# Kernel tuning notes

Measured on AMD Instinct MI355X. Metric: run time of the kernel, lower is better.

Reference implementation:

```python
import jax, jax.numpy as jnp
import numpy as np

B, T, D, H = 8, 512, 1024, 16
DH = D // H  # per-head feature dim (64)


def setup_inputs() -> dict:
    key = jax.random.key(0)
    ks = jax.random.split(key, 10)
    s = 1.0 / np.sqrt(DH)
    inp = {
        "X_data": jax.random.normal(ks[0], (B, T, D), dtype=jnp.float32),
        "mask": jnp.ones((B, T), dtype=jnp.int32),
        # per-head Q/K/V projections (each SelfAttention has its own d_h x d_h weights)
        "Wq": jax.random.normal(ks[1], (H, DH, DH), dtype=jnp.float32) * s,
        "bq": jnp.zeros((H, DH), dtype=jnp.float32),
        "Wk": jax.random.normal(ks[2], (H, DH, DH), dtype=jnp.float32) * s,
        "bk": jnp.zeros((H, DH), dtype=jnp.float32),
        "Wv": jax.random.normal(ks[3], (H, DH, DH), dtype=jnp.float32) * s,
        "bv": jnp.zeros((H, DH), dtype=jnp.float32),
        # AttentionFusion: linear on concatenated head outputs -> len_feature_new
        "Wf": jax.random.normal(ks[4], (D, D), dtype=jnp.float32) * (1.0 / np.sqrt(D)),
        "bf": jnp.zeros((D,), dtype=jnp.float32),
    }
    return inp


def reference(X_data, mask, Wq, bq, Wk, bk, Wv, bv, Wf, bf):
    # Split features into heads: [B, T, H, DH] (equal partitions since D % H == 0)
    Xh = X_data.reshape(B, T, H, DH)
    # Batched per-head projections (replaces the Python loop over heads)
    Q = jnp.einsum("bthd,hde->bhte", Xh, Wq) + bq[None, :, None, :]
    K = jnp.einsum("bthd,hde->bhte", Xh, Wk) + bk[None, :, None, :]
    V = jnp.einsum("bthd,hde->bhte", Xh, Wv) + bv[None, :, None, :]
    scale = 1.0 / jnp.sqrt(jnp.asarray(DH, dtype=Q.dtype))
    scores = jnp.einsum("bhqe,bhke->bhqk", Q, K) * scale  # [B, H, T, T]
    scores = jnp.where(mask[:, None, None, :] > 0, scores, jnp.asarray(-1e9, scores.dtype))
    att = jax.nn.softmax(scores, axis=-1)
    out = jnp.einsum("bhqk,bhke->bhqe", att, V)  # [B, H, T, DH]
    # Concatenate heads (same order as the per-head loop) and fuse
    out = out.transpose(0, 2, 1, 3).reshape(B, T, D)
    fused = out @ Wf + bf  # AttentionFusion linear
    return fused
```

## Files before the change

### kernel.cpp

```cpp
#include <hip/hip_runtime.h>
#include <math.h>

#define B 8
#define T 512
#define D 1024
#define H 16
#define DH 64

typedef __bf16 bf16;
typedef __attribute__((ext_vector_type(8))) __bf16 bf16x8;
typedef __attribute__((ext_vector_type(4))) __bf16 bf16x4;
typedef __attribute__((ext_vector_type(4))) float f32x4;

__device__ __forceinline__ void gld16(const void* g, void* l) {
    __builtin_amdgcn_global_load_lds(
        (const __attribute__((address_space(1))) void*)g,
        (__attribute__((address_space(3))) void*)l, 16, 0, 0);
}


#define EXP2SCALE 1.44269504088896f

__global__ __launch_bounds__(256) void prep_w(
    const float* __restrict__ Wq, const float* __restrict__ Wk,
    const float* __restrict__ Wv, const float* __restrict__ Wf,
    bf16* __restrict__ WqT, bf16* __restrict__ WkT,
    bf16* __restrict__ WvT, bf16* __restrict__ WfT)
{
    __shared__ bf16 Ts[64 * 72];
    const int blk = blockIdx.x, tid = threadIdx.x;
    if (blk < 48) {
        const int m = blk >> 4, h = blk & 15;
        const float* src = (m == 0 ? Wq : (m == 1 ? Wk : Wv)) + h * 4096;
        bf16* dst = (m == 0 ? WqT : (m == 1 ? WkT : WvT)) + h * 4096;
        for (int i = tid; i < 1024; i += 256) {
            const int d = i >> 4, eq = (i & 15) * 4;
            const float4 w = *(const float4*)(src + d * 64 + eq);
            Ts[(eq + 0) * 72 + d] = (bf16)w.x; Ts[(eq + 1) * 72 + d] = (bf16)w.y;
            Ts[(eq + 2) * 72 + d] = (bf16)w.z; Ts[(eq + 3) * 72 + d] = (bf16)w.w;
        }
        __syncthreads();
        for (int i = tid; i < 512; i += 256) {
            const int e = i >> 3, kc = (i & 7) * 8;
            *(bf16x8*)(dst + e * 64 + kc) = *(const bf16x8*)&Ts[e * 72 + kc];
        }
    } else {
        const int ti = blk - 48, k0 = (ti >> 4) * 64, n0 = (ti & 15) * 64;
        for (int i = tid; i < 1024; i += 256) {
            const int k = i >> 4, nq = (i & 15) * 4;
            const float4 w = *(const float4*)(Wf + (size_t)(k0 + k) * D + n0 + nq);
            Ts[(nq + 0) * 72 + k] = (bf16)w.x; Ts[(nq + 1) * 72 + k] = (bf16)w.y;
            Ts[(nq + 2) * 72 + k] = (bf16)w.z; Ts[(nq + 3) * 72 + k] = (bf16)w.w;
        }
        __syncthreads();
        for (int i = tid; i < 512; i += 256) {
            const int n = i >> 3, kc = (i & 7) * 8;
            *(bf16x8*)(WfT + (size_t)(n0 + n) * D + k0 + kc) = *(const bf16x8*)&Ts[n * 72 + kc];
        }
    }
}

__global__ __launch_bounds__(256, 2) void qkv_attn(
    const float* __restrict__ X, const int* __restrict__ mask,
    const bf16* __restrict__ WqT, const bf16* __restrict__ WkT,
    const bf16* __restrict__ WvT,
    const float* __restrict__ bq, const float* __restrict__ bk,
    const float* __restrict__ bv,
    bf16* __restrict__ Ob)
{
    __shared__ __align__(16) char smem[80384];
    bf16* Wks = (bf16*)(smem);
    bf16* Wvs = (bf16*)(smem + 8192);
    bf16* Pl  = (bf16*)(smem + 53248);
    bf16* Xkt = (bf16*)(smem + 71680);
    int*  msk = (int*)(smem + 79872);
    bf16* Wqs   = (bf16*)(smem + 16384);
    bf16* Xq    = Pl;
    bf16* Stage = Pl;
    bf16* Ostage = Pl;

    const int bh = blockIdx.x & 127, q0 = (blockIdx.x >> 7) * 128;
    const int b = bh >> 4, h = bh & 15;
    const int tid = threadIdx.x, wave = tid >> 6, lane = tid & 63;
    const int quad = lane >> 4, l15 = lane & 15;
    const int lr = lane >> 3, lc = lane & 7;
    const int csw = (lc ^ lr) * 8;
    (void)bk;

    const int pkrow = wave * 16 + (lane >> 2);
    const int pc0 = (lane & 3) * 2;

    float bqr[4], bvr[4];
#pragma unroll
    for (int nt = 0; nt < 4; ++nt) {
        bqr[nt] = bq[h * DH + nt * 16 + l15];
        bvr[nt] = bv[h * DH + nt * 16 + l15];
    }

    float4 px0, px1, px2, px3;
    {
        const float* src = X + (size_t)(b * T + pkrow) * D + h * DH + pc0 * 8;
        px0 = *(const float4*)src; px1 = *(const float4*)(src + 4);
        px2 = *(const float4*)(src + 8); px3 = *(const float4*)(src + 12);
    }
    int mreg = (tid < 64) ? mask[(size_t)b * T + tid] : 0;

    {
        const int r1 = wave * 16;
#pragma unroll
        for (int j = 0; j < 2; ++j) {
            gld16(WqT + (size_t)h * 4096 + (r1 + j * 8 + lr) * 64 + csw, &Wqs[(r1 + j * 8) * 64]);
            gld16(WkT + (size_t)h * 4096 + (r1 + j * 8 + lr) * 64 + csw, &Wks[(r1 + j * 8) * 64]);
            gld16(WvT + (size_t)h * 4096 + (r1 + j * 8 + lr) * 64 + csw, &Wvs[(r1 + j * 8) * 64]);
        }
    }
    for (int i = tid; i < 1024; i += 256) {
        const int row = i >> 3, c = i & 7;
        const float* src = X + (size_t)(b * T + q0 + row) * D + h * DH + c * 8;
        const float4 x0 = *(const float4*)src;
        const float4 x1 = *(const float4*)(src + 4);
        bf16x8 t;
        t[0] = (bf16)x0.x; t[1] = (bf16)x0.y; t[2] = (bf16)x0.z; t[3] = (bf16)x0.w;
        t[4] = (bf16)x1.x; t[5] = (bf16)x1.y; t[6] = (bf16)x1.z; t[7] = (bf16)x1.w;
        *(bf16x8*)&Xq[row * 64 + ((c ^ (row & 7)) * 8)] = t;
    }
    __syncthreads();

    {
        f32x4 accQ[2][4] = {};
#pragma unroll
        for (int ks = 0; ks < 2; ++ks) {
            bf16x8 af[2], bfr[4];
#pragma unroll
            for (int mt = 0; mt < 2; ++mt) {
                const int row = wave * 32 + mt * 16 + l15;
                af[mt] = *(const bf16x8*)&Xq[row * 64 + (((ks * 4 + quad) ^ (l15 & 7)) * 8)];
            }
#pragma unroll
            for (int nt = 0; nt < 4; ++nt)
                bfr[nt] = *(const bf16x8*)&Wqs[(nt * 16 + l15) * 64 + (((ks * 4 + quad) ^ (l15 & 7)) * 8)];
#pragma unroll
            for (int mt = 0; mt < 2; ++mt)
#pragma unroll
                for (int nt = 0; nt < 4; ++nt)
                    accQ[mt][nt] = __builtin_amdgcn_mfma_f32_16x16x32_bf16(af[mt], bfr[nt], accQ[mt][nt], 0, 0, 0);
        }
        __syncthreads();
        const float qs = 0.125f * EXP2SCALE;
#pragma unroll
        for (int mt = 0; mt < 2; ++mt)
#pragma unroll
            for (int nt = 0; nt < 4; ++nt)
#pragma unroll
                for (int reg = 0; reg < 4; ++reg)
                    Stage[(wave * 32 + mt * 16 + quad * 4 + reg) * 72 + nt * 16 + l15] =
                        (bf16)((accQ[mt][nt][reg] + bqr[nt]) * qs);
        __builtin_amdgcn_wave_barrier();
    }
    bf16x8 qf[2][2];
#pragma unroll
    for (int mt = 0; mt < 2; ++mt)
#pragma unroll
        for (int ks = 0; ks < 2; ++ks)
            qf[mt][ks] = *(const bf16x8*)&Stage[(wave * 32 + mt * 16 + l15) * 72 + ks * 32 + quad * 8];

    f32x4 acc[2][4] = {};
    float lst2[2] = {0.f, 0.f};

    for (int kt = 0; kt < 8; ++kt) {
        const int p = kt & 1;
        bf16* Ks  = (bf16*)(smem + 16384 + p * 9216);
        bf16* Vts = (bf16*)(smem + 34816 + p * 9216);

        {
            bf16x8 t0, t1;
            t0[0] = (bf16)px0.x; t0[1] = (bf16)px0.y; t0[2] = (bf16)px0.z; t0[3] = (bf16)px0.w;
            t0[4] = (bf16)px1.x; t0[5] = (bf16)px1.y; t0[6] = (bf16)px1.z; t0[7] = (bf16)px1.w;
            t1[0] = (bf16)px2.x; t1[1] = (bf16)px2.y; t1[2] = (bf16)px2.z; t1[3] = (bf16)px2.w;
            t1[4] = (bf16)px3.x; t1[5] = (bf16)px3.y; t1[6] = (bf16)px3.z; t1[7] = (bf16)px3.w;
            *(bf16x8*)&Xkt[pkrow * 64 + ((pc0 ^ (pkrow & 7)) * 8)] = t0;
            *(bf16x8*)&Xkt[pkrow * 64 + (((pc0 + 1) ^ (pkrow & 7)) * 8)] = t1;
            if (tid < 64) msk[p * 64 + tid] = mreg;
        }
        __builtin_amdgcn_wave_barrier();

        if (kt < 7) {
            const float* src = X + (size_t)(b * T + (kt + 1) * 64 + pkrow) * D + h * DH + pc0 * 8;
            px0 = *(const float4*)src; px1 = *(const float4*)(src + 4);
            px2 = *(const float4*)(src + 8); px3 = *(const float4*)(src + 12);
            if (tid < 64) mreg = mask[(size_t)b * T + (kt + 1) * 64 + tid];
        }

        {
            bf16x8 afkv[2];
#pragma unroll
            for (int ks = 0; ks < 2; ++ks)
                afkv[ks] = *(const bf16x8*)&Xkt[(wave * 16 + l15) * 64 + (((ks * 4 + quad) ^ (l15 & 7)) * 8)];
            f32x4 accK[4] = {}, accV[4] = {};
#pragma unroll
            for (int ks = 0; ks < 2; ++ks)
#pragma unroll
                for (int nt = 0; nt < 4; ++nt) {
                    const bf16x8 bk8 = *(const bf16x8*)&Wks[(nt * 16 + l15) * 64 + (((ks * 4 + quad) ^ (l15 & 7)) * 8)];
                    accK[nt] = __builtin_amdgcn_mfma_f32_16x16x32_bf16(bk8, afkv[ks], accK[nt], 0, 0, 0);
                    const bf16x8 bv8 = *(const bf16x8*)&Wvs[(nt * 16 + l15) * 64 + (((ks * 4 + quad) ^ (l15 & 7)) * 8)];
                    accV[nt] = __builtin_amdgcn_mfma_f32_16x16x32_bf16(afkv[ks], bv8, accV[nt], 0, 0, 0);
                }
#pragma unroll
            for (int nt = 0; nt < 4; ++nt) {
                bf16x4 kp;
#pragma unroll
                for (int reg = 0; reg < 4; ++reg) kp[reg] = (bf16)accK[nt][reg];
                *(bf16x4*)&Ks[(wave * 16 + l15) * 72 + nt * 16 + quad * 4] = kp;
                bf16x4 vp;
#pragma unroll
                for (int reg = 0; reg < 4; ++reg) vp[reg] = (bf16)accV[nt][reg];
                *(bf16x4*)&Vts[(nt * 16 + l15) * 72 + wave * 16 + quad * 4] = vp;
            }
        }
        __syncthreads();

        bf16* Plw = Pl + wave * (32 * 72);
        {
            bf16x8 kf[4][2];
#pragma unroll
            for (int nt = 0; nt < 4; ++nt)
#pragma unroll
                for (int ks = 0; ks < 2; ++ks)
                    kf[nt][ks] = *(const bf16x8*)&Ks[(nt * 16 + l15) * 72 + ks * 32 + quad * 8];
            int4 mv4[4];
#pragma unroll
            for (int nt = 0; nt < 4; ++nt)
                mv4[nt] = *(const int4*)&msk[p * 64 + nt * 16 + quad * 4];
#pragma unroll
            for (int mt = 0; mt < 2; ++mt) {
                f32x4 s[4] = {};
#pragma unroll
                for (int ks = 0; ks < 2; ++ks)
#pragma unroll
                    for (int nt = 0; nt < 4; ++nt)
                        s[nt] = __builtin_amdgcn_mfma_f32_16x16x32_bf16(kf[nt][ks], qf[mt][ks], s[nt], 0, 0, 0);
#pragma unroll
                for (int nt = 0; nt < 4; ++nt) {
                    bf16x4 pp;
                    const float p0 = (mv4[nt].x > 0) ? exp2f(s[nt][0]) : 0.f;
                    const float p1 = (mv4[nt].y > 0) ? exp2f(s[nt][1]) : 0.f;
                    const float p2 = (mv4[nt].z > 0) ? exp2f(s[nt][2]) : 0.f;
                    const float p3 = (mv4[nt].w > 0) ? exp2f(s[nt][3]) : 0.f;
                    lst2[mt] += (p0 + p1) + (p2 + p3);
                    pp[0] = (bf16)p0; pp[1] = (bf16)p1; pp[2] = (bf16)p2; pp[3] = (bf16)p3;
                    *(bf16x4*)&Plw[(mt * 16 + l15) * 72 + nt * 16 + quad * 4] = pp;
                }
            }
        }
        __builtin_amdgcn_wave_barrier();

#pragma unroll
        for (int kc = 0; kc < 2; ++kc) {
            const bf16x8 pf0 = *(const bf16x8*)&Plw[(l15) * 72 + kc * 32 + quad * 8];
            const bf16x8 pf1 = *(const bf16x8*)&Plw[(16 + l15) * 72 + kc * 32 + quad * 8];
#pragma unroll
            for (int nt = 0; nt < 4; ++nt) {
                const bf16x8 vf = *(const bf16x8*)&Vts[(nt * 16 + l15) * 72 + kc * 32 + quad * 8];
                acc[0][nt] = __builtin_amdgcn_mfma_f32_16x16x32_bf16(pf0, vf, acc[0][nt], 0, 0, 0);
                acc[1][nt] = __builtin_amdgcn_mfma_f32_16x16x32_bf16(pf1, vf, acc[1][nt], 0, 0, 0);
            }
        }
    }

    __builtin_amdgcn_wave_barrier();
    float inv_r[2][4];
#pragma unroll
    for (int mt = 0; mt < 2; ++mt) {
        float l = lst2[mt];
        l += __shfl_xor(l, 16);
        l += __shfl_xor(l, 32);
        const float inv = 1.f / l;
#pragma unroll
        for (int reg = 0; reg < 4; ++reg)
            inv_r[mt][reg] = __shfl(inv, (lane & 48) | (quad * 4 + reg));
    }
#pragma unroll
    for (int mt = 0; mt < 2; ++mt)
#pragma unroll
        for (int reg = 0; reg < 4; ++reg) {
            const int row = wave * 32 + mt * 16 + quad * 4 + reg;
#pragma unroll
            for (int nt = 0; nt < 4; ++nt)
                Ostage[row * 72 + nt * 16 + l15] =
                    (bf16)(acc[mt][nt][reg] * inv_r[mt][reg] + bvr[nt]);
        }
    __syncthreads();
    for (int i = tid; i < 1024; i += 256) {
        const int row = i >> 3, c = (i & 7) * 8;
        *(bf16x8*)(Ob + ((size_t)b * T + q0 + row) * D + h * DH + c) =
            *(const bf16x8*)&Ostage[row * 72 + c];
    }
}

__global__ __launch_bounds__(256, 2) void fuse_mfma(
    const bf16* __restrict__ Ob, const bf16* __restrict__ WfT,
    const float* __restrict__ bfv, float* __restrict__ out)
{
    __shared__ __align__(16) char smem[65536];

    const int col0 = blockIdx.x * 128;
    const int row0 = blockIdx.y * 128;
    const int tid = threadIdx.x, wave = tid >> 6, lane = tid & 63;
    const int quad = lane >> 4, l15 = lane & 15;
    const int lr = lane >> 3, lc = lane & 7;
    const int wm = wave * 32;

    f32x4 acc[2][8] = {};

    auto stage = [&](int k0, int buf) {
        bf16* As = (bf16*)(smem + buf * 16384);
        bf16* Bs = (bf16*)(smem + 32768 + buf * 16384);
#pragma unroll
        for (int j = 0; j < 4; ++j) {
            const int row = wm + j * 8 + lr;
            gld16(Ob + (size_t)(row0 + row) * D + k0 + ((lc ^ (row & 7)) * 8),
                  &As[(wm + j * 8) * 64]);
            gld16(WfT + (size_t)(col0 + row) * D + k0 + ((lc ^ (row & 7)) * 8),
                  &Bs[(wm + j * 8) * 64]);
        }
    };

    stage(0, 0);
    __syncthreads();

    for (int i = 0; i < 16; ++i) {
        const int buf = i & 1;
        if (i < 15) stage((i + 1) * 64, buf ^ 1);
        bf16* As = (bf16*)(smem + buf * 16384);
        bf16* Bs = (bf16*)(smem + 32768 + buf * 16384);
#pragma unroll
        for (int ks = 0; ks < 2; ++ks) {
            bf16x8 af[2], bfr[8];
#pragma unroll
            for (int mt = 0; mt < 2; ++mt) {
                const int row = wm + mt * 16 + l15;
                af[mt] = *(const bf16x8*)&As[row * 64 + (((ks * 4 + quad) ^ (l15 & 7)) * 8)];
            }
#pragma unroll
            for (int nt = 0; nt < 8; ++nt)
                bfr[nt] = *(const bf16x8*)&Bs[(nt * 16 + l15) * 64 + (((ks * 4 + quad) ^ (l15 & 7)) * 8)];
#pragma unroll
            for (int mt = 0; mt < 2; ++mt)
#pragma unroll
                for (int nt = 0; nt < 8; ++nt)
                    acc[mt][nt] = __builtin_amdgcn_mfma_f32_16x16x32_bf16(af[mt], bfr[nt], acc[mt][nt], 0, 0, 0);
        }
        __syncthreads();
    }

    float* Ofs = (float*)smem;
    float bias[8];
#pragma unroll
    for (int nt = 0; nt < 8; ++nt) bias[nt] = bfv[col0 + nt * 16 + l15];
#pragma unroll
    for (int cp = 0; cp < 2; ++cp) {
        if (cp) __syncthreads();
#pragma unroll
        for (int mt = 0; mt < 2; ++mt)
#pragma unroll
            for (int reg = 0; reg < 4; ++reg) {
                const int row = wm + mt * 16 + quad * 4 + reg;
#pragma unroll
                for (int nn = 0; nn < 4; ++nn)
                    Ofs[row * 68 + nn * 16 + l15] = acc[mt][cp * 4 + nn][reg] + bias[cp * 4 + nn];
            }
        __syncthreads();
        for (int i = tid; i < 2048; i += 256) {
            const int row = i >> 4, c = (i & 15) * 4;
            *(float4*)(out + (size_t)(row0 + row) * D + col0 + cp * 64 + c) =
                *(const float4*)&Ofs[row * 68 + c];
        }
    }
}

extern "C" void kernel_launch(void* const* d_in, const int* in_sizes, int n_in,
                              void* d_out, int out_size, void* d_ws, size_t ws_size,
                              hipStream_t stream) {
    const float* X   = (const float*)d_in[0];
    const int* mask  = (const int*)d_in[1];
    const float* Wq  = (const float*)d_in[2];
    const float* bq  = (const float*)d_in[3];
    const float* Wk  = (const float*)d_in[4];
    const float* bk  = (const float*)d_in[5];
    const float* Wv  = (const float*)d_in[6];
    const float* bv  = (const float*)d_in[7];
    const float* Wf  = (const float*)d_in[8];
    const float* bfv = (const float*)d_in[9];
    float* out = (float*)d_out;

    bf16* wsb = (bf16*)d_ws;
    const size_t QN = (size_t)B * H * T * DH;
    bf16* Ob  = wsb;
    bf16* WfT = wsb + QN;
    bf16* WqT = WfT + (size_t)D * D;
    bf16* WkT = WqT + H * DH * DH;
    bf16* WvT = WkT + H * DH * DH;

    prep_w<<<dim3(304), 256, 0, stream>>>(Wq, Wk, Wv, Wf, WqT, WkT, WvT, WfT);
    qkv_attn<<<dim3(512), 256, 0, stream>>>(X, mask, WqT, WkT, WvT, bq, bk, bv, Ob);
    fuse_mfma<<<dim3(D / 128, (B * T) / 128), 256, 0, stream>>>(Ob, WfT, bfv, out);
}
```

Before: 128.4 us.

## Precompute K/V once in prep kernel instead of per query tile

Previously each attention block recomputed the K and V projections for all 512 keys. Because there were 4 query tiles per (batch, head), that projection work was repeated 4 times. K and V are now computed once in the prep kernel and written to the workspace as bf16, with V stored transposed. The attention kernel streams them in via global_load_lds double buffering, uses 64-query tiles with 1024 blocks and higher occupancy, and loads the mask straight into registers. The fuse GEMM moves to 512 threads with a 2x4 wave split. The cost is extra global traffic for the K/V round trip and heavier prep work.

```diff
diff --git a/kernel.cpp b/kernel.cpp
--- a/kernel.cpp
+++ b/kernel.cpp
@@ -21,18 +21,20 @@
 
 #define EXP2SCALE 1.44269504088896f
 
-__global__ __launch_bounds__(256) void prep_w(
+__global__ __launch_bounds__(256) void prep(
+    const float* __restrict__ X,
     const float* __restrict__ Wq, const float* __restrict__ Wk,
     const float* __restrict__ Wv, const float* __restrict__ Wf,
-    bf16* __restrict__ WqT, bf16* __restrict__ WkT,
-    bf16* __restrict__ WvT, bf16* __restrict__ WfT)
+    bf16* __restrict__ WqT, bf16* __restrict__ WfT,
+    bf16* __restrict__ Kg, bf16* __restrict__ Vg)
 {
-    __shared__ bf16 Ts[64 * 72];
+    __shared__ __align__(16) char smemP[34816];
     const int blk = blockIdx.x, tid = threadIdx.x;
-    if (blk < 48) {
-        const int m = blk >> 4, h = blk & 15;
-        const float* src = (m == 0 ? Wq : (m == 1 ? Wk : Wv)) + h * 4096;
-        bf16* dst = (m == 0 ? WqT : (m == 1 ? WkT : WvT)) + h * 4096;
+    if (blk < 16) {
+        bf16* Ts = (bf16*)smemP;
+        const int h = blk;
+        const float* src = Wq + h * 4096;
+        bf16* dst = WqT + h * 4096;
         for (int i = tid; i < 1024; i += 256) {
             const int d = i >> 4, eq = (i & 15) * 4;
             const float4 w = *(const float4*)(src + d * 64 + eq);
@@ -44,8 +46,9 @@
             const int e = i >> 3, kc = (i & 7) * 8;
             *(bf16x8*)(dst + e * 64 + kc) = *(const bf16x8*)&Ts[e * 72 + kc];
         }
-    } else {
-        const int ti = blk - 48, k0 = (ti >> 4) * 64, n0 = (ti & 15) * 64;
+    } else if (blk < 272) {
+        bf16* Ts = (bf16*)smemP;
+        const int ti = blk - 16, k0 = (ti >> 4) * 64, n0 = (ti & 15) * 64;
         for (int i = tid; i < 1024; i += 256) {
             const int k = i >> 4, nq = (i & 15) * 4;
             const float4 w = *(const float4*)(Wf + (size_t)(k0 + k) * D + n0 + nq);
@@ -57,38 +60,92 @@
             const int n = i >> 3, kc = (i & 7) * 8;
             *(bf16x8*)(WfT + (size_t)(n0 + n) * D + k0 + kc) = *(const bf16x8*)&Ts[n * 72 + kc];
         }
+    } else {
+        const int kb_ = blk - 272;
+        const int b = kb_ >> 6, h = (kb_ >> 2) & 15, key0 = (kb_ & 3) * 128;
+        const int bh = b * 16 + h;
+        bf16* Xs  = (bf16*)smemP;
+        bf16* Wks = (bf16*)(smemP + 16384);
+        bf16* Wvs = (bf16*)(smemP + 25600);
+        const int wave = tid >> 6, lane = tid & 63;
+        const int quad = lane >> 4, l15 = lane & 15;
+        for (int i = tid; i < 1024; i += 256) {
+            const int row = i >> 3, c = i & 7;
+            const float* s4 = X + (size_t)(b * T + key0 + row) * D + h * DH + c * 8;
+            const float4 x0 = *(const float4*)s4;
+            const float4 x1 = *(const float4*)(s4 + 4);
+            bf16x8 t;
+            t[0] = (bf16)x0.x; t[1] = (bf16)x0.y; t[2] = (bf16)x0.z; t[3] = (bf16)x0.w;
+            t[4] = (bf16)x1.x; t[5] = (bf16)x1.y; t[6] = (bf16)x1.z; t[7] = (bf16)x1.w;
+            *(bf16x8*)&Xs[row * 64 + ((c ^ (row & 7)) * 8)] = t;
+        }
+        for (int i = tid; i < 1024; i += 256) {
+            const int d = i >> 4, eq = (i & 15) * 4;
+            const float4 wk4 = *(const float4*)(Wk + h * 4096 + d * 64 + eq);
+            Wks[(eq + 0) * 72 + d] = (bf16)wk4.x; Wks[(eq + 1) * 72 + d] = (bf16)wk4.y;
+            Wks[(eq + 2) * 72 + d] = (bf16)wk4.z; Wks[(eq + 3) * 72 + d] = (bf16)wk4.w;
+            const float4 wv4 = *(const float4*)(Wv + h * 4096 + d * 64 + eq);
+            Wvs[(eq + 0) * 72 + d] = (bf16)wv4.x; Wvs[(eq + 1) * 72 + d] = (bf16)wv4.y;
+            Wvs[(eq + 2) * 72 + d] = (bf16)wv4.z; Wvs[(eq + 3) * 72 + d] = (bf16)wv4.w;
+        }
+        __syncthreads();
+        bf16x8 xf[2][2];
+#pragma unroll
+        for (int kb = 0; kb < 2; ++kb)
+#pragma unroll
+            for (int ks = 0; ks < 2; ++ks)
+                xf[kb][ks] = *(const bf16x8*)&Xs[(wave * 32 + kb * 16 + l15) * 64 +
+                                                 (((ks * 4 + quad) ^ (l15 & 7)) * 8)];
+        f32x4 accK[2][4] = {}, accV[2][4] = {};
+#pragma unroll
+        for (int ks = 0; ks < 2; ++ks)
+#pragma unroll
+            for (int nt = 0; nt < 4; ++nt) {
+                const bf16x8 wk8 = *(const bf16x8*)&Wks[(nt * 16 + l15) * 72 + ks * 32 + quad * 8];
+                const bf16x8 wv8 = *(const bf16x8*)&Wvs[(nt * 16 + l15) * 72 + ks * 32 + quad * 8];
+#pragma unroll
+                for (int kb = 0; kb < 2; ++kb) {
+                    accK[kb][nt] = __builtin_amdgcn_mfma_f32_16x16x32_bf16(wk8, xf[kb][ks], accK[kb][nt], 0, 0, 0);
+                    accV[kb][nt] = __builtin_amdgcn_mfma_f32_16x16x32_bf16(xf[kb][ks], wv8, accV[kb][nt], 0, 0, 0);
+                }
+            }
+        const size_t base = (size_t)bh * 32768;
+#pragma unroll
+        for (int kb = 0; kb < 2; ++kb)
+#pragma unroll
+            for (int nt = 0; nt < 4; ++nt) {
+                const int keyK = key0 + wave * 32 + kb * 16 + l15;
+                bf16x4 kp;
+#pragma unroll
+                for (int reg = 0; reg < 4; ++reg) kp[reg] = (bf16)accK[kb][nt][reg];
+                *(bf16x4*)(Kg + base + (size_t)keyK * 64 + nt * 16 + quad * 4) = kp;
+                const int kv0 = key0 + wave * 32 + kb * 16 + quad * 4;
+                bf16x4 vp;
+#pragma unroll
+                for (int reg = 0; reg < 4; ++reg) vp[reg] = (bf16)accV[kb][nt][reg];
+                *(bf16x4*)(Vg + base + (size_t)(nt * 16 + l15) * 512 + kv0) = vp;
+            }
     }
 }
 
-__global__ __launch_bounds__(256, 2) void qkv_attn(
+__global__ __launch_bounds__(256, 4) void attn(
     const float* __restrict__ X, const int* __restrict__ mask,
-    const bf16* __restrict__ WqT, const bf16* __restrict__ WkT,
-    const bf16* __restrict__ WvT,
-    const float* __restrict__ bq, const float* __restrict__ bk,
-    const float* __restrict__ bv,
-    bf16* __restrict__ Ob)
+    const bf16* __restrict__ WqT, const float* __restrict__ bq,
+    const float* __restrict__ bv, const bf16* __restrict__ Kg,
+    const bf16* __restrict__ Vg, bf16* __restrict__ Ob)
 {
-    __shared__ __align__(16) char smem[80384];
-    bf16* Wks = (bf16*)(smem);
-    bf16* Wvs = (bf16*)(smem + 8192);
-    bf16* Pl  = (bf16*)(smem + 53248);
-    bf16* Xkt = (bf16*)(smem + 71680);
-    int*  msk = (int*)(smem + 79872);
-    bf16* Wqs   = (bf16*)(smem + 16384);
-    bf16* Xq    = Pl;
-    bf16* Stage = Pl;
-    bf16* Ostage = Pl;
-
-    const int bh = blockIdx.x & 127, q0 = (blockIdx.x >> 7) * 128;
+    __shared__ __align__(16) char smem[40960];
+    const int bh = blockIdx.x & 127, q0 = (blockIdx.x >> 7) * 64;
     const int b = bh >> 4, h = bh & 15;
     const int tid = threadIdx.x, wave = tid >> 6, lane = tid & 63;
     const int quad = lane >> 4, l15 = lane & 15;
     const int lr = lane >> 3, lc = lane & 7;
     const int csw = (lc ^ lr) * 8;
-    (void)bk;
-
-    const int pkrow = wave * 16 + (lane >> 2);
-    const int pc0 = (lane & 3) * 2;
+    const size_t kvbase = (size_t)bh * 32768;
+
+    bf16* Wqs = (bf16*)smem;
+    bf16* Xq  = (bf16*)(smem + 32768);
+    bf16* Plw = (bf16*)(smem + 32768 + wave * 2048);
 
     float bqr[4], bvr[4];
 #pragma unroll
@@ -97,24 +154,16 @@
         bvr[nt] = bv[h * DH + nt * 16 + l15];
     }
 
-    float4 px0, px1, px2, px3;
-    {
-        const float* src = X + (size_t)(b * T + pkrow) * D + h * DH + pc0 * 8;
-        px0 = *(const float4*)src; px1 = *(const float4*)(src + 4);
-        px2 = *(const float4*)(src + 8); px3 = *(const float4*)(src + 12);
-    }
-    int mreg = (tid < 64) ? mask[(size_t)b * T + tid] : 0;
-
-    {
-        const int r1 = wave * 16;
-#pragma unroll
-        for (int j = 0; j < 2; ++j) {
-            gld16(WqT + (size_t)h * 4096 + (r1 + j * 8 + lr) * 64 + csw, &Wqs[(r1 + j * 8) * 64]);
-            gld16(WkT + (size_t)h * 4096 + (r1 + j * 8 + lr) * 64 + csw, &Wks[(r1 + j * 8) * 64]);
-            gld16(WvT + (size_t)h * 4096 + (r1 + j * 8 + lr) * 64 + csw, &Wvs[(r1 + j * 8) * 64]);
-        }
-    }
-    for (int i = tid; i < 1024; i += 256) {
+    int4 mvc[4], mvn[4];
+#pragma unroll
+    for (int nt = 0; nt < 4; ++nt)
+        mvc[nt] = *(const int4*)&mask[(size_t)b * T + nt * 16 + quad * 4];
+
+#pragma unroll
+    for (int j = 0; j < 2; ++j)
+        gld16(WqT + (size_t)h * 4096 + (j * 32 + wave * 8 + lr) * 64 + csw,
+              &Wqs[(j * 32 + wave * 8) * 64]);
+    for (int i = tid; i < 512; i += 256) {
         const int row = i >> 3, c = i & 7;
         const float* src = X + (size_t)(b * T + q0 + row) * D + h * DH + c * 8;
         const float4 x0 = *(const float4*)src;
@@ -126,203 +175,149 @@
     }
     __syncthreads();
 
+    f32x4 accQ[4] = {};
+#pragma unroll
+    for (int ks = 0; ks < 2; ++ks) {
+        const bf16x8 a8 = *(const bf16x8*)&Xq[(wave * 16 + l15) * 64 + (((ks * 4 + quad) ^ (l15 & 7)) * 8)];
+#pragma unroll
+        for (int nt = 0; nt < 4; ++nt) {
+            const bf16x8 w8 = *(const bf16x8*)&Wqs[(nt * 16 + l15) * 64 + (((ks * 4 + quad) ^ (l15 & 7)) * 8)];
+            accQ[nt] = __builtin_amdgcn_mfma_f32_16x16x32_bf16(a8, w8, accQ[nt], 0, 0, 0);
+        }
+    }
+    __syncthreads();
+
     {
-        f32x4 accQ[2][4] = {};
-#pragma unroll
-        for (int ks = 0; ks < 2; ++ks) {
-            bf16x8 af[2], bfr[4];
-#pragma unroll
-            for (int mt = 0; mt < 2; ++mt) {
-                const int row = wave * 32 + mt * 16 + l15;
-                af[mt] = *(const bf16x8*)&Xq[row * 64 + (((ks * 4 + quad) ^ (l15 & 7)) * 8)];
-            }
-#pragma unroll
-            for (int nt = 0; nt < 4; ++nt)
-                bfr[nt] = *(const bf16x8*)&Wqs[(nt * 16 + l15) * 64 + (((ks * 4 + quad) ^ (l15 & 7)) * 8)];
-#pragma unroll
-            for (int mt = 0; mt < 2; ++mt)
-#pragma unroll
-                for (int nt = 0; nt < 4; ++nt)
-                    accQ[mt][nt] = __builtin_amdgcn_mfma_f32_16x16x32_bf16(af[mt], bfr[nt], accQ[mt][nt], 0, 0, 0);
-        }
-        __syncthreads();
-        const float qs = 0.125f * EXP2SCALE;
-#pragma unroll
-        for (int mt = 0; mt < 2; ++mt)
-#pragma unroll
-            for (int nt = 0; nt < 4; ++nt)
-#pragma unroll
-                for (int reg = 0; reg < 4; ++reg)
-                    Stage[(wave * 32 + mt * 16 + quad * 4 + reg) * 72 + nt * 16 + l15] =
-                        (bf16)((accQ[mt][nt][reg] + bqr[nt]) * qs);
-        __builtin_amdgcn_wave_barrier();
-    }
-    bf16x8 qf[2][2];
-#pragma unroll
-    for (int mt = 0; mt < 2; ++mt)
-#pragma unroll
-        for (int ks = 0; ks < 2; ++ks)
-            qf[mt][ks] = *(const bf16x8*)&Stage[(wave * 32 + mt * 16 + l15) * 72 + ks * 32 + quad * 8];
-
-    f32x4 acc[2][4] = {};
-    float lst2[2] = {0.f, 0.f};
+        bf16* KsL = (bf16*)smem;
+        bf16* VtL = (bf16*)(smem + 16384);
+#pragma unroll
+        for (int j = 0; j < 2; ++j) {
+            const int row = j * 32 + wave * 8 + lr;
+            gld16(Kg + kvbase + (size_t)row * 64 + csw, &KsL[(j * 32 + wave * 8) * 64]);
+            gld16(Vg + kvbase + (size_t)row * 512 + csw, &VtL[(j * 32 + wave * 8) * 64]);
+        }
+    }
+
+    const float qs = 0.125f * EXP2SCALE;
+#pragma unroll
+    for (int nt = 0; nt < 4; ++nt)
+#pragma unroll
+        for (int reg = 0; reg < 4; ++reg) {
+            const int q = quad * 4 + reg;
+            Plw[q * 64 + (((nt * 2 + (l15 >> 3)) ^ (q & 7)) * 8) + (l15 & 7)] =
+                (bf16)((accQ[nt][reg] + bqr[nt]) * qs);
+        }
+    __builtin_amdgcn_wave_barrier();
+    bf16x8 qf[2];
+#pragma unroll
+    for (int ks = 0; ks < 2; ++ks)
+        qf[ks] = *(const bf16x8*)&Plw[l15 * 64 + (((ks * 4 + quad) ^ (l15 & 7)) * 8)];
+    __builtin_amdgcn_wave_barrier();
+
+    f32x4 acc[4] = {};
+    float lsum = 0.f;
 
     for (int kt = 0; kt < 8; ++kt) {
         const int p = kt & 1;
-        bf16* Ks  = (bf16*)(smem + 16384 + p * 9216);
-        bf16* Vts = (bf16*)(smem + 34816 + p * 9216);
-
-        {
-            bf16x8 t0, t1;
-            t0[0] = (bf16)px0.x; t0[1] = (bf16)px0.y; t0[2] = (bf16)px0.z; t0[3] = (bf16)px0.w;
-            t0[4] = (bf16)px1.x; t0[5] = (bf16)px1.y; t0[6] = (bf16)px1.z; t0[7] = (bf16)px1.w;
-            t1[0] = (bf16)px2.x; t1[1] = (bf16)px2.y; t1[2] = (bf16)px2.z; t1[3] = (bf16)px2.w;
-            t1[4] = (bf16)px3.x; t1[5] = (bf16)px3.y; t1[6] = (bf16)px3.z; t1[7] = (bf16)px3.w;
-            *(bf16x8*)&Xkt[pkrow * 64 + ((pc0 ^ (pkrow & 7)) * 8)] = t0;
-            *(bf16x8*)&Xkt[pkrow * 64 + (((pc0 + 1) ^ (pkrow & 7)) * 8)] = t1;
-            if (tid < 64) msk[p * 64 + tid] = mreg;
+        __syncthreads();
+        if (kt < 7) {
+            bf16* KsL = (bf16*)(smem + (p ^ 1) * 8192);
+            bf16* VtL = (bf16*)(smem + 16384 + (p ^ 1) * 8192);
+#pragma unroll
+            for (int j = 0; j < 2; ++j) {
+                const int row = j * 32 + wave * 8 + lr;
+                gld16(Kg + kvbase + (size_t)((kt + 1) * 64 + row) * 64 + csw,
+                      &KsL[(j * 32 + wave * 8) * 64]);
+                gld16(Vg + kvbase + (size_t)row * 512 + (kt + 1) * 64 + csw,
+                      &VtL[(j * 32 + wave * 8) * 64]);
+            }
+#pragma unroll
+            for (int nt = 0; nt < 4; ++nt)
+                mvn[nt] = *(const int4*)&mask[(size_t)b * T + (kt + 1) * 64 + nt * 16 + quad * 4];
+        }
+        bf16* Ks = (bf16*)(smem + p * 8192);
+        bf16* Vt = (bf16*)(smem + 16384 + p * 8192);
+
+        f32x4 s[4] = {};
+#pragma unroll
+        for (int ks = 0; ks < 2; ++ks)
+#pragma unroll
+            for (int nt = 0; nt < 4; ++nt) {
+                const bf16x8 k8 = *(const bf16x8*)&Ks[(nt * 16 + l15) * 64 + (((ks * 4 + quad) ^ (l15 & 7)) * 8)];
+                s[nt] = __builtin_amdgcn_mfma_f32_16x16x32_bf16(k8, qf[ks], s[nt], 0, 0, 0);
+            }
+#pragma unroll
+        for (int nt = 0; nt < 4; ++nt) {
+            const float p0 = (mvc[nt].x > 0) ? exp2f(s[nt][0]) : 0.f;
+            const float p1 = (mvc[nt].y > 0) ? exp2f(s[nt][1]) : 0.f;
+            const float p2 = (mvc[nt].z > 0) ? exp2f(s[nt][2]) : 0.f;
+            const float p3 = (mvc[nt].w > 0) ? exp2f(s[nt][3]) : 0.f;
+            lsum += (p0 + p1) + (p2 + p3);
+            bf16x4 pp;
+            pp[0] = (bf16)p0; pp[1] = (bf16)p1; pp[2] = (bf16)p2; pp[3] = (bf16)p3;
+            *(bf16x4*)&Plw[l15 * 64 + (((nt * 2 + (quad >> 1)) ^ (l15 & 7)) * 8) + (quad & 1) * 4] = pp;
         }
         __builtin_amdgcn_wave_barrier();
-
-        if (kt < 7) {
-            const float* src = X + (size_t)(b * T + (kt + 1) * 64 + pkrow) * D + h * DH + pc0 * 8;
-            px0 = *(const float4*)src; px1 = *(const float4*)(src + 4);
-            px2 = *(const float4*)(src + 8); px3 = *(const float4*)(src + 12);
-            if (tid < 64) mreg = mask[(size_t)b * T + (kt + 1) * 64 + tid];
-        }
-
-        {
-            bf16x8 afkv[2];
-#pragma unroll
-            for (int ks = 0; ks < 2; ++ks)
-                afkv[ks] = *(const bf16x8*)&Xkt[(wave * 16 + l15) * 64 + (((ks * 4 + quad) ^ (l15 & 7)) * 8)];
-            f32x4 accK[4] = {}, accV[4] = {};
-#pragma unroll
-            for (int ks = 0; ks < 2; ++ks)
-#pragma unroll
-                for (int nt = 0; nt < 4; ++nt) {
-                    const bf16x8 bk8 = *(const bf16x8*)&Wks[(nt * 16 + l15) * 64 + (((ks * 4 + quad) ^ (l15 & 7)) * 8)];
-                    accK[nt] = __builtin_amdgcn_mfma_f32_16x16x32_bf16(bk8, afkv[ks], accK[nt], 0, 0, 0);
-                    const bf16x8 bv8 = *(const bf16x8*)&Wvs[(nt * 16 + l15) * 64 + (((ks * 4 + quad) ^ (l15 & 7)) * 8)];
-                    accV[nt] = __builtin_amdgcn_mfma_f32_16x16x32_bf16(afkv[ks], bv8, accV[nt], 0, 0, 0);
-                }
+#pragma unroll
+        for (int kc = 0; kc < 2; ++kc) {
+            const bf16x8 pf = *(const bf16x8*)&Plw[l15 * 64 + (((kc * 4 + quad) ^ (l15 & 7)) * 8)];
 #pragma unroll
             for (int nt = 0; nt < 4; ++nt) {
-                bf16x4 kp;
-#pragma unroll
-                for (int reg = 0; reg < 4; ++reg) kp[reg] = (bf16)accK[nt][reg];
-                *(bf16x4*)&Ks[(wave * 16 + l15) * 72 + nt * 16 + quad * 4] = kp;
-                bf16x4 vp;
-#pragma unroll
-                for (int reg = 0; reg < 4; ++reg) vp[reg] = (bf16)accV[nt][reg];
-                *(bf16x4*)&Vts[(nt * 16 + l15) * 72 + wave * 16 + quad * 4] = vp;
+                const bf16x8 vf = *(const bf16x8*)&Vt[(nt * 16 + l15) * 64 + (((kc * 4 + quad) ^ (l15 & 7)) * 8)];
+                acc[nt] = __builtin_amdgcn_mfma_f32_16x16x32_bf16(pf, vf, acc[nt], 0, 0, 0);
             }
         }
-        __syncthreads();
-
-        bf16* Plw = Pl + wave * (32 * 72);
-        {
-            bf16x8 kf[4][2];
-#pragma unroll
-            for (int nt = 0; nt < 4; ++nt)
-#pragma unroll
-                for (int ks = 0; ks < 2; ++ks)
-                    kf[nt][ks] = *(const bf16x8*)&Ks[(nt * 16 + l15) * 72 + ks * 32 + quad * 8];
-            int4 mv4[4];
-#pragma unroll
-            for (int nt = 0; nt < 4; ++nt)
-                mv4[nt] = *(const int4*)&msk[p * 64 + nt * 16 + quad * 4];
-#pragma unroll
-            for (int mt = 0; mt < 2; ++mt) {
-                f32x4 s[4] = {};
-#pragma unroll
-                for (int ks = 0; ks < 2; ++ks)
-#pragma unroll
-                    for (int nt = 0; nt < 4; ++nt)
-                        s[nt] = __builtin_amdgcn_mfma_f32_16x16x32_bf16(kf[nt][ks], qf[mt][ks], s[nt], 0, 0, 0);
-#pragma unroll
-                for (int nt = 0; nt < 4; ++nt) {
-                    bf16x4 pp;
-                    const float p0 = (mv4[nt].x > 0) ? exp2f(s[nt][0]) : 0.f;
-                    const float p1 = (mv4[nt].y > 0) ? exp2f(s[nt][1]) : 0.f;
-                    const float p2 = (mv4[nt].z > 0) ? exp2f(s[nt][2]) : 0.f;
-                    const float p3 = (mv4[nt].w > 0) ? exp2f(s[nt][3]) : 0.f;
-                    lst2[mt] += (p0 + p1) + (p2 + p3);
-                    pp[0] = (bf16)p0; pp[1] = (bf16)p1; pp[2] = (bf16)p2; pp[3] = (bf16)p3;
-                    *(bf16x4*)&Plw[(mt * 16 + l15) * 72 + nt * 16 + quad * 4] = pp;
-                }
-            }
-        }
-        __builtin_amdgcn_wave_barrier();
-
-#pragma unroll
-        for (int kc = 0; kc < 2; ++kc) {
-            const bf16x8 pf0 = *(const bf16x8*)&Plw[(l15) * 72 + kc * 32 + quad * 8];
-            const bf16x8 pf1 = *(const bf16x8*)&Plw[(16 + l15) * 72 + kc * 32 + quad * 8];
-#pragma unroll
-            for (int nt = 0; nt < 4; ++nt) {
-                const bf16x8 vf = *(const bf16x8*)&Vts[(nt * 16 + l15) * 72 + kc * 32 + quad * 8];
-                acc[0][nt] = __builtin_amdgcn_mfma_f32_16x16x32_bf16(pf0, vf, acc[0][nt], 0, 0, 0);
-                acc[1][nt] = __builtin_amdgcn_mfma_f32_16x16x32_bf16(pf1, vf, acc[1][nt], 0, 0, 0);
-            }
-        }
-    }
-
-    __builtin_amdgcn_wave_barrier();
-    float inv_r[2][4];
-#pragma unroll
-    for (int mt = 0; mt < 2; ++mt) {
-        float l = lst2[mt];
-        l += __shfl_xor(l, 16);
-        l += __shfl_xor(l, 32);
-        const float inv = 1.f / l;
+#pragma unroll
+        for (int nt = 0; nt < 4; ++nt) mvc[nt] = mvn[nt];
+    }
+
+    __syncthreads();
+    float l = lsum;
+    l += __shfl_xor(l, 16);
+    l += __shfl_xor(l, 32);
+    const float inv = 1.f / l;
+    float inv_r[4];
+#pragma unroll
+    for (int reg = 0; reg < 4; ++reg)
+        inv_r[reg] = __shfl(inv, (lane & 48) | (quad * 4 + reg));
+    bf16* Ostage = (bf16*)smem;
+#pragma unroll
+    for (int nt = 0; nt < 4; ++nt)
 #pragma unroll
         for (int reg = 0; reg < 4; ++reg)
-            inv_r[mt][reg] = __shfl(inv, (lane & 48) | (quad * 4 + reg));
-    }
-#pragma unroll
-    for (int mt = 0; mt < 2; ++mt)
-#pragma unroll
-        for (int reg = 0; reg < 4; ++reg) {
-            const int row = wave * 32 + mt * 16 + quad * 4 + reg;
-#pragma unroll
-            for (int nt = 0; nt < 4; ++nt)
-                Ostage[row * 72 + nt * 16 + l15] =
-                    (bf16)(acc[mt][nt][reg] * inv_r[mt][reg] + bvr[nt]);
-        }
+            Ostage[(wave * 16 + quad * 4 + reg) * 72 + nt * 16 + l15] =
+                (bf16)(acc[nt][reg] * inv_r[reg] + bvr[nt]);
     __syncthreads();
-    for (int i = tid; i < 1024; i += 256) {
+    for (int i = tid; i < 512; i += 256) {
         const int row = i >> 3, c = (i & 7) * 8;
         *(bf16x8*)(Ob + ((size_t)b * T + q0 + row) * D + h * DH + c) =
             *(const bf16x8*)&Ostage[row * 72 + c];
     }
 }
 
-__global__ __launch_bounds__(256, 2) void fuse_mfma(
+__global__ __launch_bounds__(512, 2) void fuse_mfma(
     const bf16* __restrict__ Ob, const bf16* __restrict__ WfT,
     const float* __restrict__ bfv, float* __restrict__ out)
 {
     __shared__ __align__(16) char smem[65536];
-
     const int col0 = blockIdx.x * 128;
     const int row0 = blockIdx.y * 128;
     const int tid = threadIdx.x, wave = tid >> 6, lane = tid & 63;
     const int quad = lane >> 4, l15 = lane & 15;
     const int lr = lane >> 3, lc = lane & 7;
-    const int wm = wave * 32;
-
-    f32x4 acc[2][8] = {};
+    const int csw = (lc ^ lr) * 8;
+    const int wm = (wave >> 1) * 32, wn = (wave & 1) * 64;
+
+    f32x4 acc[2][4] = {};
 
     auto stage = [&](int k0, int buf) {
         bf16* As = (bf16*)(smem + buf * 16384);
         bf16* Bs = (bf16*)(smem + 32768 + buf * 16384);
 #pragma unroll
-        for (int j = 0; j < 4; ++j) {
-            const int row = wm + j * 8 + lr;
-            gld16(Ob + (size_t)(row0 + row) * D + k0 + ((lc ^ (row & 7)) * 8),
-                  &As[(wm + j * 8) * 64]);
-            gld16(WfT + (size_t)(col0 + row) * D + k0 + ((lc ^ (row & 7)) * 8),
-                  &Bs[(wm + j * 8) * 64]);
+        for (int j = 0; j < 2; ++j) {
+            const int row = j * 64 + wave * 8 + lr;
+            gld16(Ob + (size_t)(row0 + row) * D + k0 + csw, &As[(j * 64 + wave * 8) * 64]);
+            gld16(WfT + (size_t)(col0 + row) * D + k0 + csw, &Bs[(j * 64 + wave * 8) * 64]);
         }
     };
 
@@ -336,42 +331,42 @@
         bf16* Bs = (bf16*)(smem + 32768 + buf * 16384);
 #pragma unroll
         for (int ks = 0; ks < 2; ++ks) {
-            bf16x8 af[2], bfr[8];
-#pragma unroll
-            for (int mt = 0; mt < 2; ++mt) {
-                const int row = wm + mt * 16 + l15;
-                af[mt] = *(const bf16x8*)&As[row * 64 + (((ks * 4 + quad) ^ (l15 & 7)) * 8)];
-            }
-#pragma unroll
-            for (int nt = 0; nt < 8; ++nt)
-                bfr[nt] = *(const bf16x8*)&Bs[(nt * 16 + l15) * 64 + (((ks * 4 + quad) ^ (l15 & 7)) * 8)];
+            bf16x8 af[2], bfr[4];
 #pragma unroll
             for (int mt = 0; mt < 2; ++mt)
-#pragma unroll
-                for (int nt = 0; nt < 8; ++nt)
+                af[mt] = *(const bf16x8*)&As[(wm + mt * 16 + l15) * 64 + (((ks * 4 + quad) ^ (l15 & 7)) * 8)];
+#pragma unroll
+            for (int nt = 0; nt < 4; ++nt)
+                bfr[nt] = *(const bf16x8*)&Bs[(wn + nt * 16 + l15) * 64 + (((ks * 4 + quad) ^ (l15 & 7)) * 8)];
+#pragma unroll
+            for (int mt = 0; mt < 2; ++mt)
+#pragma unroll
+                for (int nt = 0; nt < 4; ++nt)
                     acc[mt][nt] = __builtin_amdgcn_mfma_f32_16x16x32_bf16(af[mt], bfr[nt], acc[mt][nt], 0, 0, 0);
         }
         __syncthreads();
     }
 
     float* Ofs = (float*)smem;
-    float bias[8];
-#pragma unroll
-    for (int nt = 0; nt < 8; ++nt) bias[nt] = bfv[col0 + nt * 16 + l15];
+    float bias[4];
+#pragma unroll
+    for (int nt = 0; nt < 4; ++nt) bias[nt] = bfv[col0 + wn + nt * 16 + l15];
 #pragma unroll
     for (int cp = 0; cp < 2; ++cp) {
         if (cp) __syncthreads();
-#pragma unroll
-        for (int mt = 0; mt < 2; ++mt)
-#pragma unroll
-            for (int reg = 0; reg < 4; ++reg) {
-                const int row = wm + mt * 16 + quad * 4 + reg;
-#pragma unroll
-                for (int nn = 0; nn < 4; ++nn)
-                    Ofs[row * 68 + nn * 16 + l15] = acc[mt][cp * 4 + nn][reg] + bias[cp * 4 + nn];
-            }
-        __syncthreads();
-        for (int i = tid; i < 2048; i += 256) {
+        if ((wave & 1) == cp) {
+#pragma unroll
+            for (int mt = 0; mt < 2; ++mt)
+#pragma unroll
+                for (int reg = 0; reg < 4; ++reg) {
+                    const int row = wm + mt * 16 + quad * 4 + reg;
+#pragma unroll
+                    for (int nt = 0; nt < 4; ++nt)
+                        Ofs[row * 68 + nt * 16 + l15] = acc[mt][nt][reg] + bias[nt];
+                }
+        }
+        __syncthreads();
+        for (int i = tid; i < 2048; i += 512) {
             const int row = i >> 4, c = (i & 15) * 4;
             *(float4*)(out + (size_t)(row0 + row) * D + col0 + cp * 64 + c) =
                 *(const float4*)&Ofs[row * 68 + c];
@@ -393,16 +388,17 @@
     const float* Wf  = (const float*)d_in[8];
     const float* bfv = (const float*)d_in[9];
     float* out = (float*)d_out;
+    (void)bk;
 
     bf16* wsb = (bf16*)d_ws;
     const size_t QN = (size_t)B * H * T * DH;
     bf16* Ob  = wsb;
     bf16* WfT = wsb + QN;
     bf16* WqT = WfT + (size_t)D * D;
-    bf16* WkT = WqT + H * DH * DH;
-    bf16* WvT = WkT + H * DH * DH;
-
-    prep_w<<<dim3(304), 256, 0, stream>>>(Wq, Wk, Wv, Wf, WqT, WkT, WvT, WfT);
-    qkv_attn<<<dim3(512), 256, 0, stream>>>(X, mask, WqT, WkT, WvT, bq, bk, bv, Ob);
-    fuse_mfma<<<dim3(D / 128, (B * T) / 128), 256, 0, stream>>>(Ob, WfT, bfv, out);
+    bf16* Kg  = WqT + (size_t)H * DH * DH;
+    bf16* Vg  = Kg + QN;
+
+    prep<<<dim3(784), 256, 0, stream>>>(X, Wq, Wk, Wv, Wf, WqT, WfT, Kg, Vg);
+    attn<<<dim3(1024), 256, 0, stream>>>(X, mask, WqT, bq, bv, Kg, Vg, Ob);
+    fuse_mfma<<<dim3(D / 128, (B * T) / 128), 512, 0, stream>>>(Ob, WfT, bfv, out);
 }
```

Result: slower. 133.8 us (+4.2%).

## Fold weight prep into attention kernel, converting per-head weights in-block

Applied to the files above, without the earlier changes.

Removes the separate prep_w launch. The Wf transpose-to-bf16 work now runs in 256 extra blocks appended to the qkv_attn grid, and each attention block loads its own head's fp32 Wq/Wk/Wv, converts them, and writes them transposed and swizzled into LDS. This saves one kernel launch and the global round trip for the per-head weights. In exchange every one of the 512 attention blocks now re-reads and converts its weights with scalar 2-byte LDS stores instead of async 16-byte global-to-LDS loads.

```diff
diff --git a/kernel.cpp b/kernel.cpp
--- a/kernel.cpp
+++ b/kernel.cpp
@@ -21,31 +21,20 @@
 
 #define EXP2SCALE 1.44269504088896f
 
-__global__ __launch_bounds__(256) void prep_w(
+__global__ __launch_bounds__(256, 2) void qkv_attn(
+    const float* __restrict__ X, const int* __restrict__ mask,
     const float* __restrict__ Wq, const float* __restrict__ Wk,
-    const float* __restrict__ Wv, const float* __restrict__ Wf,
-    bf16* __restrict__ WqT, bf16* __restrict__ WkT,
-    bf16* __restrict__ WvT, bf16* __restrict__ WfT)
+    const float* __restrict__ Wv,
+    const float* __restrict__ bq, const float* __restrict__ bv,
+    const float* __restrict__ Wf, bf16* __restrict__ WfT,
+    bf16* __restrict__ Ob)
 {
-    __shared__ bf16 Ts[64 * 72];
-    const int blk = blockIdx.x, tid = threadIdx.x;
-    if (blk < 48) {
-        const int m = blk >> 4, h = blk & 15;
-        const float* src = (m == 0 ? Wq : (m == 1 ? Wk : Wv)) + h * 4096;
-        bf16* dst = (m == 0 ? WqT : (m == 1 ? WkT : WvT)) + h * 4096;
-        for (int i = tid; i < 1024; i += 256) {
-            const int d = i >> 4, eq = (i & 15) * 4;
-            const float4 w = *(const float4*)(src + d * 64 + eq);
-            Ts[(eq + 0) * 72 + d] = (bf16)w.x; Ts[(eq + 1) * 72 + d] = (bf16)w.y;
-            Ts[(eq + 2) * 72 + d] = (bf16)w.z; Ts[(eq + 3) * 72 + d] = (bf16)w.w;
-        }
-        __syncthreads();
-        for (int i = tid; i < 512; i += 256) {
-            const int e = i >> 3, kc = (i & 7) * 8;
-            *(bf16x8*)(dst + e * 64 + kc) = *(const bf16x8*)&Ts[e * 72 + kc];
-        }
-    } else {
-        const int ti = blk - 48, k0 = (ti >> 4) * 64, n0 = (ti & 15) * 64;
+    __shared__ __align__(16) char smem[80384];
+
+    if (blockIdx.x >= 512) {
+        bf16* Ts = (bf16*)smem;
+        const int ti = blockIdx.x - 512, tid = threadIdx.x;
+        const int k0 = (ti >> 4) * 64, n0 = (ti & 15) * 64;
         for (int i = tid; i < 1024; i += 256) {
             const int k = i >> 4, nq = (i & 15) * 4;
             const float4 w = *(const float4*)(Wf + (size_t)(k0 + k) * D + n0 + nq);
@@ -57,18 +46,9 @@
             const int n = i >> 3, kc = (i & 7) * 8;
             *(bf16x8*)(WfT + (size_t)(n0 + n) * D + k0 + kc) = *(const bf16x8*)&Ts[n * 72 + kc];
         }
-    }
-}
-
-__global__ __launch_bounds__(256, 2) void qkv_attn(
-    const float* __restrict__ X, const int* __restrict__ mask,
-    const bf16* __restrict__ WqT, const bf16* __restrict__ WkT,
-    const bf16* __restrict__ WvT,
-    const float* __restrict__ bq, const float* __restrict__ bk,
-    const float* __restrict__ bv,
-    bf16* __restrict__ Ob)
-{
-    __shared__ __align__(16) char smem[80384];
+        return;
+    }
+
     bf16* Wks = (bf16*)(smem);
     bf16* Wvs = (bf16*)(smem + 8192);
     bf16* Pl  = (bf16*)(smem + 53248);
@@ -83,9 +63,6 @@
     const int b = bh >> 4, h = bh & 15;
     const int tid = threadIdx.x, wave = tid >> 6, lane = tid & 63;
     const int quad = lane >> 4, l15 = lane & 15;
-    const int lr = lane >> 3, lc = lane & 7;
-    const int csw = (lc ^ lr) * 8;
-    (void)bk;
 
     const int pkrow = wave * 16 + (lane >> 2);
     const int pc0 = (lane & 3) * 2;
@@ -105,14 +82,21 @@
     }
     int mreg = (tid < 64) ? mask[(size_t)b * T + tid] : 0;
 
-    {
-        const int r1 = wave * 16;
-#pragma unroll
-        for (int j = 0; j < 2; ++j) {
-            gld16(WqT + (size_t)h * 4096 + (r1 + j * 8 + lr) * 64 + csw, &Wqs[(r1 + j * 8) * 64]);
-            gld16(WkT + (size_t)h * 4096 + (r1 + j * 8 + lr) * 64 + csw, &Wks[(r1 + j * 8) * 64]);
-            gld16(WvT + (size_t)h * 4096 + (r1 + j * 8 + lr) * 64 + csw, &Wvs[(r1 + j * 8) * 64]);
-        }
+    for (int i = tid; i < 1024; i += 256) {
+        const int d = i >> 4, eq4 = (i & 15) * 4;
+        const int cw = ((d >> 3)) * 8 + (d & 7);
+        const float4 wq4 = *(const float4*)(Wq + (size_t)h * 4096 + d * 64 + eq4);
+        const float4 wk4 = *(const float4*)(Wk + (size_t)h * 4096 + d * 64 + eq4);
+        const float4 wv4 = *(const float4*)(Wv + (size_t)h * 4096 + d * 64 + eq4);
+#pragma unroll
+        for (int j = 0; j < 4; ++j) {
+            const int e = eq4 + j;
+            const int idx = e * 64 + (((d >> 3) ^ (e & 7)) * 8) + (d & 7);
+            Wqs[idx] = (bf16)((const float*)&wq4)[j];
+            Wks[idx] = (bf16)((const float*)&wk4)[j];
+            Wvs[idx] = (bf16)((const float*)&wv4)[j];
+        }
+        (void)cw;
     }
     for (int i = tid; i < 1024; i += 256) {
         const int row = i >> 3, c = i & 7;
@@ -393,16 +377,13 @@
     const float* Wf  = (const float*)d_in[8];
     const float* bfv = (const float*)d_in[9];
     float* out = (float*)d_out;
+    (void)bk;
 
     bf16* wsb = (bf16*)d_ws;
     const size_t QN = (size_t)B * H * T * DH;
     bf16* Ob  = wsb;
     bf16* WfT = wsb + QN;
-    bf16* WqT = WfT + (size_t)D * D;
-    bf16* WkT = WqT + H * DH * DH;
-    bf16* WvT = WkT + H * DH * DH;
-
-    prep_w<<<dim3(304), 256, 0, stream>>>(Wq, Wk, Wv, Wf, WqT, WkT, WvT, WfT);
-    qkv_attn<<<dim3(512), 256, 0, stream>>>(X, mask, WqT, WkT, WvT, bq, bk, bv, Ob);
+
+    qkv_attn<<<dim3(768), 256, 0, stream>>>(X, mask, Wq, Wk, Wv, bq, bv, Wf, WfT, Ob);
     fuse_mfma<<<dim3(D / 128, (B * T) / 128), 256, 0, stream>>>(Ob, WfT, bfv, out);
 }
```

Measured after the change: 126.0 us. About the same (-1.9%).
